# Performance work log

Hardware: AMD Instinct MI355X
Metric: run time of the kernel (lower is better)

The kernel has to match this reference:

```python
import jax, jax.numpy as jnp
import numpy as np

D_MODEL = 2048
NUM_HEADS = 32
NUM_KV_HEADS = 8
HEAD_DIM = D_MODEL // NUM_HEADS  # 64
GROUP = NUM_HEADS // NUM_KV_HEADS  # 4


def setup_inputs() -> dict:
    key = jax.random.key(0)
    ks = jax.random.split(key, 9)
    s = 1.0 / np.sqrt(D_MODEL)
    kv_dim = NUM_KV_HEADS * HEAD_DIM
    return {
        "x": jax.random.normal(ks[0], (2, 2048, D_MODEL), dtype=jnp.float32),
        "Wq": jax.random.normal(ks[1], (D_MODEL, D_MODEL), dtype=jnp.float32) * s,
        "bq": jnp.zeros((D_MODEL,), dtype=jnp.float32),
        "Wk": jax.random.normal(ks[2], (D_MODEL, kv_dim), dtype=jnp.float32) * s,
        "bk": jnp.zeros((kv_dim,), dtype=jnp.float32),
        "Wv": jax.random.normal(ks[3], (D_MODEL, kv_dim), dtype=jnp.float32) * s,
        "bv": jnp.zeros((kv_dim,), dtype=jnp.float32),
        "Wo": jax.random.normal(ks[4], (D_MODEL, D_MODEL), dtype=jnp.float32) * s,
        "bo": jnp.zeros((D_MODEL,), dtype=jnp.float32),
    }


def reference(x, Wq, bq, Wk, bk, Wv, bv, Wo, bo):
    B, S, _ = x.shape
    # projections
    q = (x @ Wq + bq).reshape(B, S, NUM_HEADS, HEAD_DIM).transpose(0, 2, 1, 3)      # [B,H,S,Dh]
    k = (x @ Wk + bk).reshape(B, S, NUM_KV_HEADS, HEAD_DIM).transpose(0, 2, 1, 3)   # [B,Hkv,S,Dh]
    v = (x @ Wv + bv).reshape(B, S, NUM_KV_HEADS, HEAD_DIM).transpose(0, 2, 1, 3)
    # expand KV heads to match query heads (repeat_interleave along head dim)
    k = jnp.repeat(k, GROUP, axis=1)  # [B,H,S,Dh]
    v = jnp.repeat(v, GROUP, axis=1)
    scale = 1.0 / np.sqrt(HEAD_DIM).astype(np.float32)
    scores = jnp.einsum('bhqd,bhkd->bhqk', q, k) * scale  # [B,H,S,S]
    attn = jax.nn.softmax(scores, axis=-1)
    out = jnp.einsum('bhqk,bhkd->bhqd', attn, v)          # [B,H,S,Dh]
    out = out.transpose(0, 2, 1, 3).reshape(B, S, NUM_HEADS * HEAD_DIM)
    return out @ Wo + bo
```

## Files before the change

kernel.cpp:

```cpp
#include <hip/hip_runtime.h>
#include <stdint.h>

typedef unsigned short u16;
typedef unsigned int u32;
typedef short bf16x8 __attribute__((ext_vector_type(8)));
typedef float f32x4 __attribute__((ext_vector_type(4)));
typedef u32 u32x2 __attribute__((ext_vector_type(2)));

#define GLOAD_LDS16(gptr, lptr)                                                \
  __builtin_amdgcn_global_load_lds(                                            \
      (__attribute__((address_space(1))) void*)(gptr),                         \
      (__attribute__((address_space(3))) void*)(lptr), 16, 0, 0)

#if __has_builtin(__builtin_amdgcn_exp2f)
#define EXP2F(x) __builtin_amdgcn_exp2f(x)
#else
#define EXP2F(x) exp2f(x)
#endif

__device__ __forceinline__ u16 f2bf(float f) {
  union { float f; uint32_t u; } v; v.f = f;
  return (u16)((v.u + 0x7fffu + ((v.u >> 16) & 1u)) >> 16);
}
__device__ __forceinline__ float bf2f(u16 h) {
  union { uint32_t u; float f; } v; v.u = ((uint32_t)h) << 16;
  return v.f;
}
__device__ __forceinline__ u32 cvt_pk_bf16(float lo, float hi) {
  u32 r;
  asm("v_cvt_pk_bf16_f32 %0, %1, %2" : "=v"(r) : "v"(lo), "v"(hi));
  return r;
}

__global__ void k_conv_bf16(const float* __restrict__ src, u16* __restrict__ dst, int n8) {
  int i = blockIdx.x * blockDim.x + threadIdx.x;
  if (i >= n8) return;
  const float4* s = (const float4*)src + (size_t)i * 2;
  float4 a = s[0], b = s[1];
  uint4 o;
  o.x = (uint32_t)f2bf(a.x) | ((uint32_t)f2bf(a.y) << 16);
  o.y = (uint32_t)f2bf(a.z) | ((uint32_t)f2bf(a.w) << 16);
  o.z = (uint32_t)f2bf(b.x) | ((uint32_t)f2bf(b.y) << 16);
  o.w = (uint32_t)f2bf(b.z) | ((uint32_t)f2bf(b.w) << 16);
  ((uint4*)dst)[i] = o;
}

__global__ void k_transpose_bf16(const float* __restrict__ src, u16* __restrict__ dst,
                                 int R, int C) {
  __shared__ float tile[32][33];
  int cb = blockIdx.x * 32, rb = blockIdx.y * 32;
  int tx = threadIdx.x, ty = threadIdx.y;
#pragma unroll
  for (int j = 0; j < 4; ++j)
    tile[ty + j * 8][tx] = src[(size_t)(rb + ty + j * 8) * C + cb + tx];
  __syncthreads();
#pragma unroll
  for (int j = 0; j < 4; ++j)
    dst[(size_t)(cb + ty + j * 8) * R + rb + tx] = f2bf(tile[tx][ty + j * 8]);
}

__global__ void k_transpose_v(const u16* __restrict__ cqkv, u16* __restrict__ vt) {
  __shared__ u16 tile[32][34];
  int st = blockIdx.x, dt = blockIdx.y, bk = blockIdx.z;
  int b = bk >> 3, kvh = bk & 7;
  int tx = threadIdx.x, ty = threadIdx.y;
  const u16* src = cqkv + (size_t)(b * 2048 + st * 32) * 3072 + 2560 + kvh * 64 + dt * 32;
#pragma unroll
  for (int j = 0; j < 4; ++j)
    tile[ty + j * 8][tx] = src[(size_t)(ty + j * 8) * 3072 + tx];
  __syncthreads();
  u16* dst = vt + ((size_t)(bk * 64 + dt * 32)) * 2048 + st * 32;
#pragma unroll
  for (int j = 0; j < 4; ++j)
    dst[(size_t)(ty + j * 8) * 2048 + tx] = tile[tx][ty + j * 8];
}

template <bool BF16OUT>
__global__ __launch_bounds__(256) void k_gemm_bt(
    const u16* __restrict__ A, const u16* __restrict__ Bt,
    const float* __restrict__ bias, void* __restrict__ Cptr,
    int M, int N, int K) {
  __shared__ u16 As[128 * 32];
  __shared__ u16 Bs[128 * 32];
  const int t = threadIdx.x;
  const int lane = t & 63;
  const int w = t >> 6, wr = w >> 1, wc = w & 1;
  const int brow = blockIdx.y * 128, bcol = blockIdx.x * 128;
  const int g = lane >> 4, q = lane & 15;

  f32x4 acc[4][4] = {};
  const int srow = t >> 2;
  const int sj = t & 3;
  const int nkt = K >> 5;
  for (int kt = 0; kt < nkt; ++kt) {
    __syncthreads();
#pragma unroll
    for (int i = 0; i < 2; ++i) {
      int row = srow + i * 64;
      int jsrc = sj ^ ((row >> 1) & 3);
      const u16* ga = A + (size_t)(brow + row) * K + kt * 32 + jsrc * 8;
      const u16* gb = Bt + (size_t)(bcol + row) * K + kt * 32 + jsrc * 8;
      GLOAD_LDS16(ga, (char*)As + i * 4096 + t * 16);
      GLOAD_LDS16(gb, (char*)Bs + i * 4096 + t * 16);
    }
    __syncthreads();
    bf16x8 a[4], b[4];
#pragma unroll
    for (int mt = 0; mt < 4; ++mt) {
      int row = wr * 64 + mt * 16 + q;
      int pos = g ^ ((row >> 1) & 3);
      a[mt] = *(const bf16x8*)(As + row * 32 + pos * 8);
    }
#pragma unroll
    for (int nt = 0; nt < 4; ++nt) {
      int row = wc * 64 + nt * 16 + q;
      int pos = g ^ ((row >> 1) & 3);
      b[nt] = *(const bf16x8*)(Bs + row * 32 + pos * 8);
    }
#pragma unroll
    for (int mt = 0; mt < 4; ++mt)
#pragma unroll
      for (int nt = 0; nt < 4; ++nt)
        acc[mt][nt] = __builtin_amdgcn_mfma_f32_16x16x32_bf16(a[mt], b[nt], acc[mt][nt], 0, 0, 0);
  }
#pragma unroll
  for (int nt = 0; nt < 4; ++nt) {
    int col = bcol + wc * 64 + nt * 16 + q;
    float bv_ = bias[col];
#pragma unroll
    for (int mt = 0; mt < 4; ++mt) {
#pragma unroll
      for (int r = 0; r < 4; ++r) {
        int row = brow + wr * 64 + mt * 16 + g * 4 + r;
        float val = acc[mt][nt][r] + bv_;
        if (BF16OUT)
          ((u16*)Cptr)[(size_t)row * N + col] = f2bf(val);
        else
          ((float*)Cptr)[(size_t)row * N + col] = val;
      }
    }
  }
}

#define LOG2E 1.44269504088896340736f
__global__ __launch_bounds__(256) void k_attn(const u16* __restrict__ qkv,
                                              const u16* __restrict__ vt,
                                              u16* __restrict__ out) {
  const int qt = blockIdx.x, h = blockIdx.y, b = blockIdx.z;
  const int kvh = h >> 2;
  const int t = threadIdx.x, lane = t & 63, w = t >> 6;
  const int g = lane >> 4, q16 = lane & 15;
  const int LDQ = 3072;

  __shared__ u16 Ksh[2][64 * 64];
  __shared__ u16 Vsh[2][64 * 64];
  __shared__ u16 Psh[4][16 * 72] __attribute__((aligned(16)));

  bf16x8 qf[2][2];
#pragma unroll
  for (int sub = 0; sub < 2; ++sub) {
    const size_t qrow = (size_t)(b * 2048 + qt * 128 + sub * 64 + w * 16 + q16);
#pragma unroll
    for (int c = 0; c < 2; ++c) {
      bf16x8 tmp = *(const bf16x8*)(qkv + qrow * LDQ + h * 64 + c * 32 + g * 8);
#pragma unroll
      for (int i = 0; i < 8; ++i)
        tmp[i] = (short)f2bf(bf2f((u16)tmp[i]) * 0.125f);
      qf[sub][c] = tmp;
    }
  }

  f32x4 acc[2][4] = {};
  float m_run[2], l_run[2];
  m_run[0] = m_run[1] = -__builtin_inff();
  l_run[0] = l_run[1] = 0.f;

  const int kbase = b * 2048;
  const int koff = 2048 + kvh * 64;
  const u16* vtb = vt + (size_t)((b * 8 + kvh) * 64) * 2048;
  const int srow = t >> 3;
  const int sj = t & 7;

  auto stage = [&](int bb, int kt_) {
#pragma unroll
    for (int p = 0; p < 2; ++p) {
      int row = srow + p * 32;
      int cx = sj ^ (row & 7);
      const u16* gk = qkv + (size_t)(kbase + kt_ * 64 + row) * LDQ + koff + cx * 8;
      GLOAD_LDS16(gk, (char*)Ksh[bb] + p * 4096 + t * 16);
      const u16* gv = vtb + (size_t)row * 2048 + kt_ * 64 + cx * 8;
      GLOAD_LDS16(gv, (char*)Vsh[bb] + p * 4096 + t * 16);
    }
  };

  stage(0, 0);
  __syncthreads();
  int cur = 0;

  for (int kt = 0; kt < 32; ++kt) {
    if (kt < 31) stage(cur ^ 1, kt + 1);
    const u16* Kc = Ksh[cur];
    const u16* Vc = Vsh[cur];

    f32x4 sc[2][4] = {};
    __builtin_amdgcn_s_setprio(1);
#pragma unroll
    for (int c = 0; c < 2; ++c) {
#pragma unroll
      for (int nt = 0; nt < 4; ++nt) {
        int row = nt * 16 + q16;
        bf16x8 kf = *(const bf16x8*)(Kc + row * 64 + (((c * 4 + g) ^ (row & 7)) << 3));
        sc[0][nt] = __builtin_amdgcn_mfma_f32_16x16x32_bf16(kf, qf[0][c], sc[0][nt], 0, 0, 0);
        sc[1][nt] = __builtin_amdgcn_mfma_f32_16x16x32_bf16(kf, qf[1][c], sc[1][nt], 0, 0, 0);
      }
    }
    __builtin_amdgcn_s_setprio(0);

    bf16x8 pf[2][2];
#pragma unroll
    for (int sub = 0; sub < 2; ++sub) {
      float mt_ = sc[sub][0][0];
#pragma unroll
      for (int nt = 0; nt < 4; ++nt)
#pragma unroll
        for (int r = 0; r < 4; ++r)
          mt_ = fmaxf(mt_, sc[sub][nt][r]);
      mt_ = fmaxf(mt_, __shfl_xor(mt_, 16, 64));
      mt_ = fmaxf(mt_, __shfl_xor(mt_, 32, 64));
      if (__any(mt_ > m_run[sub])) {
        float mn = fmaxf(m_run[sub], mt_);
        float alpha = EXP2F((m_run[sub] - mn) * LOG2E);
        m_run[sub] = mn;
        l_run[sub] *= alpha;
#pragma unroll
        for (int r = 0; r < 4; ++r) {
          float ar = __shfl(alpha, g * 4 + r, 64);
#pragma unroll
          for (int dt = 0; dt < 4; ++dt) acc[sub][dt][r] *= ar;
        }
      }
      float mL = m_run[sub] * LOG2E;
      float lt = 0.f;
#pragma unroll
      for (int nt = 0; nt < 4; ++nt)
#pragma unroll
        for (int r = 0; r < 4; ++r) {
          float p_ = EXP2F(fmaf(sc[sub][nt][r], LOG2E, -mL));
          sc[sub][nt][r] = p_;
          lt += p_;
        }
      lt += __shfl_xor(lt, 16, 64);
      lt += __shfl_xor(lt, 32, 64);
      l_run[sub] += lt;
      u16* prow = &Psh[w][q16 * 72];
#pragma unroll
      for (int nt = 0; nt < 4; ++nt) {
        u32x2 pk;
        pk.x = cvt_pk_bf16(sc[sub][nt][0], sc[sub][nt][1]);
        pk.y = cvt_pk_bf16(sc[sub][nt][2], sc[sub][nt][3]);
        *(u32x2*)(prow + nt * 16 + g * 4) = pk;
      }
      pf[sub][0] = *(const bf16x8*)(&Psh[w][q16 * 72 + g * 8]);
      pf[sub][1] = *(const bf16x8*)(&Psh[w][q16 * 72 + 32 + g * 8]);
    }

    __builtin_amdgcn_s_setprio(1);
#pragma unroll
    for (int c = 0; c < 2; ++c) {
      int kc = c * 4 + g;
#pragma unroll
      for (int dt = 0; dt < 4; ++dt) {
        int d = dt * 16 + q16;
        bf16x8 vf = *(const bf16x8*)(Vc + d * 64 + ((kc ^ (d & 7)) << 3));
        acc[0][dt] = __builtin_amdgcn_mfma_f32_16x16x32_bf16(pf[0][c], vf, acc[0][dt], 0, 0, 0);
        acc[1][dt] = __builtin_amdgcn_mfma_f32_16x16x32_bf16(pf[1][c], vf, acc[1][dt], 0, 0, 0);
      }
    }
    __builtin_amdgcn_s_setprio(0);

    __syncthreads();
    cur ^= 1;
  }

#pragma unroll
  for (int sub = 0; sub < 2; ++sub)
#pragma unroll
    for (int r = 0; r < 4; ++r) {
      float linv = 1.0f / __shfl(l_run[sub], g * 4 + r, 64);
      size_t orow = (size_t)(b * 2048 + qt * 128 + sub * 64 + w * 16 + g * 4 + r);
#pragma unroll
      for (int dt = 0; dt < 4; ++dt)
        out[orow * 2048 + h * 64 + dt * 16 + q16] = f2bf(acc[sub][dt][r] * linv);
    }
}

extern "C" void kernel_launch(void* const* d_in, const int* in_sizes, int n_in,
                              void* d_out, int out_size, void* d_ws, size_t ws_size,
                              hipStream_t stream) {
  const float* x  = (const float*)d_in[0];
  const float* Wq = (const float*)d_in[1];
  const float* bq = (const float*)d_in[2];
  const float* Wk = (const float*)d_in[3];
  const float* bk = (const float*)d_in[4];
  const float* Wv = (const float*)d_in[5];
  const float* bv = (const float*)d_in[6];
  const float* Wo = (const float*)d_in[7];
  const float* bo = (const float*)d_in[8];
  float* out = (float*)d_out;

  char* ws = (char*)d_ws;
  u16*   xb    = (u16*)(ws + 0);
  u16*   wqkvT = (u16*)(ws + 16777216);
  u16*   woT   = (u16*)(ws + 29360128);
  float* bqkv  = (float*)(ws + 37748736);
  u16*   cqkv  = (u16*)(ws + 37761024);
  u16*   aout  = (u16*)(ws + 62926848);
  u16*   vtb   = xb;
  (void)ws_size; (void)in_sizes; (void)n_in; (void)out_size;

  hipMemcpyAsync(bqkv, bq, 2048 * sizeof(float), hipMemcpyDeviceToDevice, stream);
  hipMemcpyAsync(bqkv + 2048, bk, 512 * sizeof(float), hipMemcpyDeviceToDevice, stream);
  hipMemcpyAsync(bqkv + 2560, bv, 512 * sizeof(float), hipMemcpyDeviceToDevice, stream);

  k_conv_bf16<<<4096, 256, 0, stream>>>(x, xb, 1048576);
  dim3 tb(32, 8);
  k_transpose_bf16<<<dim3(64, 64), tb, 0, stream>>>(Wq, wqkvT, 2048, 2048);
  k_transpose_bf16<<<dim3(16, 64), tb, 0, stream>>>(Wk, wqkvT + 2048 * 2048, 2048, 512);
  k_transpose_bf16<<<dim3(16, 64), tb, 0, stream>>>(Wv, wqkvT + 2560 * 2048, 2048, 512);
  k_transpose_bf16<<<dim3(64, 64), tb, 0, stream>>>(Wo, woT, 2048, 2048);

  k_gemm_bt<true><<<dim3(24, 32), 256, 0, stream>>>(xb, wqkvT, bqkv, cqkv, 4096, 3072, 2048);
  k_transpose_v<<<dim3(64, 2, 16), tb, 0, stream>>>(cqkv, vtb);
  k_attn<<<dim3(16, 32, 2), 256, 0, stream>>>(cqkv, vtb, aout);
  k_gemm_bt<false><<<dim3(16, 32), 256, 0, stream>>>(aout, woT, bo, out, 4096, 2048, 2048);
}
```

Measured before the change: 397.9 us.

## Double-buffer GEMM LDS tiles and swizzle block order across XCDs

The bf16 GEMM kernel now double-buffers its A/B shared-memory tiles, issuing the next K-tile's global-to-LDS loads before computing the current one, and drops one barrier per iteration. It raises wave priority around the MFMA block. It also launches a 1D grid and remaps block IDs so consecutive tiles land on the same XCD (8-way interleave) for better L2 reuse. The cost is twice the LDS per block, which may lower occupancy.

```diff
diff --git a/kernel.cpp b/kernel.cpp
--- a/kernel.cpp
+++ b/kernel.cpp
@@ -79,49 +79,65 @@
 __global__ __launch_bounds__(256) void k_gemm_bt(
     const u16* __restrict__ A, const u16* __restrict__ Bt,
     const float* __restrict__ bias, void* __restrict__ Cptr,
-    int M, int N, int K) {
-  __shared__ u16 As[128 * 32];
-  __shared__ u16 Bs[128 * 32];
+    int M, int N, int K, int gx, int nwg) {
+  __shared__ u16 As[2][128 * 32];
+  __shared__ u16 Bs[2][128 * 32];
   const int t = threadIdx.x;
   const int lane = t & 63;
   const int w = t >> 6, wr = w >> 1, wc = w & 1;
-  const int brow = blockIdx.y * 128, bcol = blockIdx.x * 128;
+  const int bid = blockIdx.x;
+  const int cpx = nwg >> 3;
+  const int swz = (bid & 7) * cpx + (bid >> 3);
+  const int brow = (swz / gx) * 128, bcol = (swz % gx) * 128;
   const int g = lane >> 4, q = lane & 15;
 
   f32x4 acc[4][4] = {};
   const int srow = t >> 2;
   const int sj = t & 3;
   const int nkt = K >> 5;
-  for (int kt = 0; kt < nkt; ++kt) {
-    __syncthreads();
+
+  auto stage = [&](int bb, int kt_) {
 #pragma unroll
     for (int i = 0; i < 2; ++i) {
       int row = srow + i * 64;
       int jsrc = sj ^ ((row >> 1) & 3);
-      const u16* ga = A + (size_t)(brow + row) * K + kt * 32 + jsrc * 8;
-      const u16* gb = Bt + (size_t)(bcol + row) * K + kt * 32 + jsrc * 8;
-      GLOAD_LDS16(ga, (char*)As + i * 4096 + t * 16);
-      GLOAD_LDS16(gb, (char*)Bs + i * 4096 + t * 16);
-    }
-    __syncthreads();
+      const u16* ga = A + (size_t)(brow + row) * K + kt_ * 32 + jsrc * 8;
+      const u16* gb = Bt + (size_t)(bcol + row) * K + kt_ * 32 + jsrc * 8;
+      GLOAD_LDS16(ga, (char*)(&As[bb][0]) + i * 4096 + t * 16);
+      GLOAD_LDS16(gb, (char*)(&Bs[bb][0]) + i * 4096 + t * 16);
+    }
+  };
+
+  stage(0, 0);
+  __syncthreads();
+  int cur = 0;
+
+  for (int kt = 0; kt < nkt; ++kt) {
+    if (kt < nkt - 1) stage(cur ^ 1, kt + 1);
+    const u16* Ac = As[cur];
+    const u16* Bc = Bs[cur];
     bf16x8 a[4], b[4];
 #pragma unroll
     for (int mt = 0; mt < 4; ++mt) {
       int row = wr * 64 + mt * 16 + q;
       int pos = g ^ ((row >> 1) & 3);
-      a[mt] = *(const bf16x8*)(As + row * 32 + pos * 8);
+      a[mt] = *(const bf16x8*)(Ac + row * 32 + pos * 8);
     }
 #pragma unroll
     for (int nt = 0; nt < 4; ++nt) {
       int row = wc * 64 + nt * 16 + q;
       int pos = g ^ ((row >> 1) & 3);
-      b[nt] = *(const bf16x8*)(Bs + row * 32 + pos * 8);
-    }
+      b[nt] = *(const bf16x8*)(Bc + row * 32 + pos * 8);
+    }
+    __builtin_amdgcn_s_setprio(1);
 #pragma unroll
     for (int mt = 0; mt < 4; ++mt)
 #pragma unroll
       for (int nt = 0; nt < 4; ++nt)
         acc[mt][nt] = __builtin_amdgcn_mfma_f32_16x16x32_bf16(a[mt], b[nt], acc[mt][nt], 0, 0, 0);
+    __builtin_amdgcn_s_setprio(0);
+    __syncthreads();
+    cur ^= 1;
   }
 #pragma unroll
   for (int nt = 0; nt < 4; ++nt) {
@@ -187,9 +203,9 @@
       int row = srow + p * 32;
       int cx = sj ^ (row & 7);
       const u16* gk = qkv + (size_t)(kbase + kt_ * 64 + row) * LDQ + koff + cx * 8;
-      GLOAD_LDS16(gk, (char*)Ksh[bb] + p * 4096 + t * 16);
+      GLOAD_LDS16(gk, (char*)(&Ksh[bb][0]) + p * 4096 + t * 16);
       const u16* gv = vtb + (size_t)row * 2048 + kt_ * 64 + cx * 8;
-      GLOAD_LDS16(gv, (char*)Vsh[bb] + p * 4096 + t * 16);
+      GLOAD_LDS16(gv, (char*)(&Vsh[bb][0]) + p * 4096 + t * 16);
     }
   };
 
@@ -329,8 +345,8 @@
   k_transpose_bf16<<<dim3(16, 64), tb, 0, stream>>>(Wv, wqkvT + 2560 * 2048, 2048, 512);
   k_transpose_bf16<<<dim3(64, 64), tb, 0, stream>>>(Wo, woT, 2048, 2048);
 
-  k_gemm_bt<true><<<dim3(24, 32), 256, 0, stream>>>(xb, wqkvT, bqkv, cqkv, 4096, 3072, 2048);
+  k_gemm_bt<true><<<768, 256, 0, stream>>>(xb, wqkvT, bqkv, cqkv, 4096, 3072, 2048, 24, 768);
   k_transpose_v<<<dim3(64, 2, 16), tb, 0, stream>>>(cqkv, vtb);
   k_attn<<<dim3(16, 32, 2), 256, 0, stream>>>(cqkv, vtb, aout);
-  k_gemm_bt<false><<<dim3(16, 32), 256, 0, stream>>>(aout, woT, bo, out, 4096, 2048, 2048);
-}
+  k_gemm_bt<false><<<512, 256, 0, stream>>>(aout, woT, bo, out, 4096, 2048, 2048, 16, 512);
+}
```

Result: faster. 380.3 us (-4.4%).
